# Kernel optimization log

Hardware: AMD Instinct MI355X
Metric: run time of the kernel (lower is better)

The kernel has to match this reference:

```python
import jax, jax.numpy as jnp
import numpy as np

N = 100000
E = 1600000
IN_DIM = 256
HID = 128
HEADS = 8
DH = HID // HEADS  # 16
NCLS = 64
SLOPE = 0.2  # DGL GATConv default negative_slope


def gat_layer(h_in, W, al, ar, b, src, dst, n_nodes, heads, dh, activate):
    # per-node linear transform -> [N, H, D]
    h = (h_in @ W).reshape(n_nodes, heads, dh)
    el = jnp.sum(h * al, axis=-1)  # [N, H]
    er = jnp.sum(h * ar, axis=-1)  # [N, H]
    e = jax.nn.leaky_relu(el[src] + er[dst], SLOPE)  # [E, H]
    # edge softmax over incoming edges of each dst node (numerically stable)
    m = jax.ops.segment_max(e, dst, num_segments=n_nodes)  # [N, H]
    m = jnp.where(jnp.isfinite(m), m, jnp.zeros_like(m))  # zero-in-degree nodes
    p = jnp.exp(e - m[dst])
    s = jax.ops.segment_sum(p, dst, num_segments=n_nodes)  # [N, H]
    alpha = p / s[dst]  # [E, H]
    # gather src features, weight by attention, scatter-add to dst
    msg = h[src] * alpha[..., None]  # [E, H, D]
    out = jax.ops.segment_sum(msg, dst, num_segments=n_nodes)  # [N, H, D]
    out = out + b.reshape(1, heads, dh)
    return jax.nn.elu(out) if activate else out


def setup_inputs() -> dict:
    key = jax.random.key(0)
    ks = jax.random.split(key, 12)
    x = jax.random.normal(ks[0], (N, IN_DIM), dtype=jnp.float32)
    src = jax.random.randint(ks[1], (E,), 0, N, dtype=jnp.int32)
    dst = jax.random.randint(ks[2], (E,), 0, N, dtype=jnp.int32)
    s1 = 1.0 / np.sqrt(IN_DIM)
    s2 = 1.0 / np.sqrt(HID)
    W1 = jax.random.normal(ks[3], (IN_DIM, HID), dtype=jnp.float32) * s1
    al1 = jax.random.normal(ks[4], (HEADS, DH), dtype=jnp.float32) * s2
    ar1 = jax.random.normal(ks[5], (HEADS, DH), dtype=jnp.float32) * s2
    b1 = jnp.zeros((HID,), dtype=jnp.float32)
    W2 = jax.random.normal(ks[6], (HID, NCLS), dtype=jnp.float32) * s2
    al2 = jax.random.normal(ks[7], (1, NCLS), dtype=jnp.float32) * s2
    ar2 = jax.random.normal(ks[8], (1, NCLS), dtype=jnp.float32) * s2
    b2 = jnp.zeros((NCLS,), dtype=jnp.float32)
    return {"x": x, "src": src, "dst": dst, "W1": W1, "al1": al1, "ar1": ar1,
            "b1": b1, "W2": W2, "al2": al2, "ar2": ar2, "b2": b2}


def reference(x, src, dst, W1, al1, ar1, b1, W2, al2, ar2, b2):
    # Layer 1: 8-head GATConv with internal ELU activation
    h = gat_layer(x, W1, al1, ar1, b1, src, dst, N, HEADS, DH, activate=True)
    h = h.reshape(N, HID)  # concat heads
    h = jax.nn.elu(h)       # outer ELU (dropout is identity in eval)
    # Layer 2: single-head GATConv, no activation; mean over head dim
    out = gat_layer(h, W2, al2, ar2, b2, src, dst, N, 1, NCLS, activate=False)
    return out.mean(axis=1)  # [N, NCLS]
```

## Files before the change

### kernel.cpp

```cpp
#include <hip/hip_runtime.h>
#include <hip/hip_bf16.h>
#include <cstdint>
#include <cstddef>

#define NNODES 100000
#define NEDGES 1600000
#define IN_DIM 256
#define HID 128
#define HEADS 8
#define DH 16
#define NCLS 64
#define SLOPE 0.2f

#define NBUCK 391
#define BCAP 5120
#define EPB 4000
#define NBBLK 400

typedef __attribute__((ext_vector_type(8))) short bf16x8;
typedef __attribute__((ext_vector_type(4))) float f32x4;

static __device__ __forceinline__ unsigned short f2bf(float f) {
    __hip_bfloat16 h = __float2bfloat16(f);
    unsigned short r;
    __builtin_memcpy(&r, &h, sizeof(r));
    return r;
}
static __device__ __forceinline__ float bflo(unsigned int w) {
    union { uint32_t u; float f; } c; c.u = w << 16; return c.f;
}
static __device__ __forceinline__ float bfhi(unsigned int w) {
    union { uint32_t u; float f; } c; c.u = w & 0xFFFF0000u; return c.f;
}

__global__ __launch_bounds__(256) void prep_w1t_kernel(const float* __restrict__ W1,
                                                       short* __restrict__ W1T) {
    int idx = blockIdx.x * 256 + threadIdx.x;
    if (idx >= IN_DIM * HID) return;
    int k = idx >> 7;
    int n = idx & 127;
    W1T[n * IN_DIM + k] = (short)f2bf(W1[idx]);
}

__global__ __launch_bounds__(256) void prep_w2t_kernel(const float* __restrict__ W2,
                                                       short* __restrict__ W2T) {
    int idx = blockIdx.x * 256 + threadIdx.x;
    if (idx >= HID * NCLS) return;
    int k = idx >> 6;
    int n = idx & 63;
    W2T[n * HID + k] = (short)f2bf(W2[idx]);
}

__global__ __launch_bounds__(256) void gemm1_kernel(const float* __restrict__ x,
                                                    const short* __restrict__ W1T,
                                                    unsigned short* __restrict__ h1b) {
    __shared__ short Asl[128 * 40];
    const int tid = threadIdx.x;
    const int brow = blockIdx.x * 128;
    const int wid = tid >> 6, lane = tid & 63;
    const int wm = (wid >> 1) * 64, wn = (wid & 1) * 64;
    const int mr = lane & 15;
    const int ks = lane >> 4;
    const int sr = tid >> 1;
    const int sch = tid & 1;
    const int grow = brow + sr;
    const bool rowok = grow < NNODES;
    const float* xrow = x + (size_t)grow * IN_DIM + sch * 16;

    f32x4 acc[4][4];
#pragma unroll
    for (int i = 0; i < 4; ++i)
#pragma unroll
        for (int j = 0; j < 4; ++j) acc[i][j] = (f32x4){0.f, 0.f, 0.f, 0.f};

    float4 v0 = {0,0,0,0}, v1 = {0,0,0,0}, v2 = {0,0,0,0}, v3 = {0,0,0,0};
    if (rowok) {
        v0 = *(const float4*)(xrow + 0);
        v1 = *(const float4*)(xrow + 4);
        v2 = *(const float4*)(xrow + 8);
        v3 = *(const float4*)(xrow + 12);
    }

    for (int k0 = 0; k0 < IN_DIM; k0 += 32) {
        bf16x8 p0, p1;
        p0[0] = (short)f2bf(v0.x); p0[1] = (short)f2bf(v0.y);
        p0[2] = (short)f2bf(v0.z); p0[3] = (short)f2bf(v0.w);
        p0[4] = (short)f2bf(v1.x); p0[5] = (short)f2bf(v1.y);
        p0[6] = (short)f2bf(v1.z); p0[7] = (short)f2bf(v1.w);
        p1[0] = (short)f2bf(v2.x); p1[1] = (short)f2bf(v2.y);
        p1[2] = (short)f2bf(v2.z); p1[3] = (short)f2bf(v2.w);
        p1[4] = (short)f2bf(v3.x); p1[5] = (short)f2bf(v3.y);
        p1[6] = (short)f2bf(v3.z); p1[7] = (short)f2bf(v3.w);
        if (k0 + 32 < IN_DIM && rowok) {
            v0 = *(const float4*)(xrow + k0 + 32 + 0);
            v1 = *(const float4*)(xrow + k0 + 32 + 4);
            v2 = *(const float4*)(xrow + k0 + 32 + 8);
            v3 = *(const float4*)(xrow + k0 + 32 + 12);
        }
        __syncthreads();
        *(bf16x8*)(Asl + sr * 40 + sch * 16 + 0) = p0;
        *(bf16x8*)(Asl + sr * 40 + sch * 16 + 8) = p1;
        __syncthreads();

        bf16x8 af[4], bfr[4];
#pragma unroll
        for (int i = 0; i < 4; ++i)
            af[i] = *(const bf16x8*)(Asl + (wm + i * 16 + mr) * 40 + ks * 8);
#pragma unroll
        for (int j = 0; j < 4; ++j)
            bfr[j] = *(const bf16x8*)(W1T + (size_t)(wn + j * 16 + mr) * IN_DIM + k0 + ks * 8);
#pragma unroll
        for (int i = 0; i < 4; ++i)
#pragma unroll
            for (int j = 0; j < 4; ++j)
                acc[i][j] = __builtin_amdgcn_mfma_f32_16x16x32_bf16(af[i], bfr[j], acc[i][j], 0, 0, 0);
    }

#pragma unroll
    for (int i = 0; i < 4; ++i) {
#pragma unroll
        for (int j = 0; j < 4; ++j) {
            int col = wn + j * 16 + mr;
#pragma unroll
            for (int r = 0; r < 4; ++r) {
                int row = brow + wm + i * 16 + ks * 4 + r;
                if (row < NNODES) h1b[(size_t)row * HID + col] = f2bf(acc[i][j][r]);
            }
        }
    }
}

__global__ __launch_bounds__(256) void gemm2_kernel(const unsigned short* __restrict__ hfb,
                                                    const short* __restrict__ W2T,
                                                    const float* __restrict__ al2,
                                                    const float* __restrict__ ar2,
                                                    unsigned short* __restrict__ h2b,
                                                    float* __restrict__ el2,
                                                    float* __restrict__ er2) {
    __shared__ short A[128 * 136];
    const int tid = threadIdx.x;
    const int brow = blockIdx.x * 128;
    {
        int r = tid >> 1, half = tid & 1;
        int grow = brow + r;
        uint4* lp = (uint4*)(A + r * 136 + half * 64);
        if (grow < NNODES) {
            const uint4* gp = (const uint4*)(hfb + (size_t)grow * HID + half * 64);
#pragma unroll
            for (int i = 0; i < 8; ++i) lp[i] = gp[i];
        } else {
            uint4 z = {0, 0, 0, 0};
#pragma unroll
            for (int i = 0; i < 8; ++i) lp[i] = z;
        }
    }
    __syncthreads();

    const int wid = tid >> 6, lane = tid & 63;
    const int mr = lane & 15, ks = lane >> 4;
    const int wrow = wid * 32;

    f32x4 acc[2][4];
#pragma unroll
    for (int i = 0; i < 2; ++i)
#pragma unroll
        for (int j = 0; j < 4; ++j) acc[i][j] = (f32x4){0.f, 0.f, 0.f, 0.f};

#pragma unroll
    for (int kk = 0; kk < 4; ++kk) {
        const int k0 = kk * 32;
        bf16x8 af[2], bfr[4];
#pragma unroll
        for (int i = 0; i < 2; ++i)
            af[i] = *(const bf16x8*)(A + (wrow + i * 16 + mr) * 136 + k0 + ks * 8);
#pragma unroll
        for (int j = 0; j < 4; ++j)
            bfr[j] = *(const bf16x8*)(W2T + (size_t)(j * 16 + mr) * HID + k0 + ks * 8);
#pragma unroll
        for (int i = 0; i < 2; ++i)
#pragma unroll
            for (int j = 0; j < 4; ++j)
                acc[i][j] = __builtin_amdgcn_mfma_f32_16x16x32_bf16(af[i], bfr[j], acc[i][j], 0, 0, 0);
    }

    float al2v[4], ar2v[4];
#pragma unroll
    for (int j = 0; j < 4; ++j) { al2v[j] = al2[j * 16 + mr]; ar2v[j] = ar2[j * 16 + mr]; }

    float pl[2][4] = {}, pr[2][4] = {};
#pragma unroll
    for (int i = 0; i < 2; ++i) {
#pragma unroll
        for (int j = 0; j < 4; ++j) {
#pragma unroll
            for (int r = 0; r < 4; ++r) {
                float vvv = acc[i][j][r];
                pl[i][r] = fmaf(vvv, al2v[j], pl[i][r]);
                pr[i][r] = fmaf(vvv, ar2v[j], pr[i][r]);
                int row = brow + wrow + i * 16 + ks * 4 + r;
                if (row < NNODES) h2b[(size_t)row * NCLS + j * 16 + mr] = f2bf(vvv);
            }
        }
    }
#pragma unroll
    for (int d = 1; d <= 8; d <<= 1) {
#pragma unroll
        for (int i = 0; i < 2; ++i)
#pragma unroll
            for (int r = 0; r < 4; ++r) {
                pl[i][r] += __shfl_xor(pl[i][r], d, 64);
                pr[i][r] += __shfl_xor(pr[i][r], d, 64);
            }
    }
    if (mr == 0) {
#pragma unroll
        for (int i = 0; i < 2; ++i)
#pragma unroll
            for (int r = 0; r < 4; ++r) {
                int row = brow + wrow + i * 16 + ks * 4 + r;
                if (row < NNODES) { el2[row] = pl[i][r]; er2[row] = pr[i][r]; }
            }
    }
}

__global__ __launch_bounds__(256) void init_gcur_kernel(int* __restrict__ gcur) {
    int b = blockIdx.x * 256 + threadIdx.x;
    if (b < NBUCK) gcur[b] = b * BCAP;
}

__global__ __launch_bounds__(256) void bucket_scatter_kernel(const int* __restrict__ src,
                                                             const int* __restrict__ dst,
                                                             int* __restrict__ gcur,
                                                             unsigned* __restrict__ pairs) {
    __shared__ int cnt[NBUCK];
    __shared__ int base[NBUCK];
    const int tid = threadIdx.x;
    for (int i = tid; i < NBUCK; i += 256) cnt[i] = 0;
    __syncthreads();
    const int eb = blockIdx.x * EPB;
    for (int i = tid; i < EPB; i += 256) atomicAdd(&cnt[dst[eb + i] >> 8], 1);
    __syncthreads();
    for (int b = tid; b < NBUCK; b += 256) {
        int c = cnt[b];
        base[b] = c ? atomicAdd(&gcur[b], c) : 0;
        cnt[b] = 0;
    }
    __syncthreads();
    for (int i = tid; i < EPB; i += 256) {
        int d = dst[eb + i], s = src[eb + i];
        int b = d >> 8;
        int p = base[b] + atomicAdd(&cnt[b], 1);
        pairs[p] = ((unsigned)(d & 255) << 24) | (unsigned)s;
    }
}

__global__ __launch_bounds__(256) void bucket_csr_kernel(const unsigned* __restrict__ pairs,
                                                         const int* __restrict__ gcur,
                                                         int* __restrict__ row_off,
                                                         int* __restrict__ row_cnt,
                                                         int* __restrict__ sorted_src) {
    __shared__ int ncnt[256];
    __shared__ int nbase[256];
    __shared__ int ws[4];
    const int tid = threadIdx.x, lane = tid & 63, wid = tid >> 6;
    const int b = blockIdx.x;
    const int nbeg = b << 8;
    const int ebeg = b * BCAP;
    const int eend = gcur[b];

    ncnt[tid] = 0;
    __syncthreads();
    for (int pos = ebeg + tid; pos < eend; pos += 256)
        atomicAdd(&ncnt[pairs[pos] >> 24], 1);
    __syncthreads();
    int v = ncnt[tid];
    int x = v;
#pragma unroll
    for (int d = 1; d < 64; d <<= 1) {
        int y = __shfl_up(x, d, 64);
        if (lane >= d) x += y;
    }
    if (lane == 63) ws[wid] = x;
    __syncthreads();
    int woff = 0;
#pragma unroll
    for (int i = 0; i < 4; ++i) if (i < wid) woff += ws[i];
    int gb = ebeg + woff + (x - v);
    int node = nbeg + tid;
    if (node < NNODES) { row_off[node] = gb; row_cnt[node] = v; }
    nbase[tid] = gb;
    ncnt[tid] = 0;
    __syncthreads();
    for (int pos = ebeg + tid; pos < eend; pos += 256) {
        unsigned pr = pairs[pos];
        int l = pr >> 24;
        int p = nbase[l] + atomicAdd(&ncnt[l], 1);
        sorted_src[p] = (int)(pr & 0xFFFFFFu);
    }
}

__global__ __launch_bounds__(256) void attn_scores_kernel(const unsigned short* __restrict__ h1b,
                                                          const float* __restrict__ al,
                                                          const float* __restrict__ ar,
                                                          float* __restrict__ el,
                                                          float* __restrict__ er) {
    int idx = blockIdx.x * 256 + threadIdx.x;
    if (idx >= NNODES * HEADS) return;
    int hd = idx & (HEADS - 1);
    const uint4* hp = (const uint4*)(h1b + (size_t)idx * DH);
    uint4 A = hp[0], B = hp[1];
    unsigned int w[8] = {A.x, A.y, A.z, A.w, B.x, B.y, B.z, B.w};
    float a = 0.f, c = 0.f;
#pragma unroll
    for (int i = 0; i < 8; ++i) {
        float lo = bflo(w[i]), hi = bfhi(w[i]);
        a = fmaf(lo, al[hd * DH + 2 * i], a);
        a = fmaf(hi, al[hd * DH + 2 * i + 1], a);
        c = fmaf(lo, ar[hd * DH + 2 * i], c);
        c = fmaf(hi, ar[hd * DH + 2 * i + 1], c);
    }
    el[idx] = a;
    er[idx] = c;
}

__global__ __launch_bounds__(256) void aggregate1_kernel(const unsigned short* __restrict__ h1b,
                                                         const float* __restrict__ el1,
                                                         const float* __restrict__ er1,
                                                         const int* __restrict__ row_off,
                                                         const int* __restrict__ row_cnt,
                                                         const int* __restrict__ sorted_src,
                                                         const float* __restrict__ b1,
                                                         unsigned short* __restrict__ hfb) {
    __shared__ float b1s[HID];
    const int tid = threadIdx.x;
    if (tid < HID) b1s[tid] = b1[tid];
    __syncthreads();

    const int wid = tid >> 6, lane = tid & 63;
    const int g = lane >> 4, sub = lane & 15, hd = sub >> 1;

    for (int v = blockIdx.x * 4 + wid; v < NNODES; v += gridDim.x * 4) {
        const int beg = row_off[v];
        const int end = beg + row_cnt[v];
        const float er_v = er1[v * HEADS + hd];
        float a[8] = {0.f, 0.f, 0.f, 0.f, 0.f, 0.f, 0.f, 0.f};
        float sp = 0.f;
        for (int j0 = beg; j0 < end; j0 += 64) {
            const int nj = min(64, end - j0);
            const int nit = (nj + 3) >> 2;
            int us = (j0 + lane < end) ? sorted_src[j0 + lane] : 0;
            for (int ib = 0; ib < nit; ib += 4) {
                int j0i = g + 4 * (ib + 0), j1i = g + 4 * (ib + 1);
                int j2i = g + 4 * (ib + 2), j3i = g + 4 * (ib + 3);
                int u0 = __shfl(us, j0i, 64);
                int u1 = __shfl(us, j1i, 64);
                int u2 = __shfl(us, j2i, 64);
                int u3 = __shfl(us, j3i, 64);
                uint4 w0 = *(const uint4*)(h1b + ((unsigned)(u0 << 7) + sub * 8));
                uint4 w1 = *(const uint4*)(h1b + ((unsigned)(u1 << 7) + sub * 8));
                uint4 w2 = *(const uint4*)(h1b + ((unsigned)(u2 << 7) + sub * 8));
                uint4 w3 = *(const uint4*)(h1b + ((unsigned)(u3 << 7) + sub * 8));
                float e0 = el1[(unsigned)(u0 << 3) + hd];
                float e1 = el1[(unsigned)(u1 << 3) + hd];
                float e2 = el1[(unsigned)(u2 << 3) + hd];
                float e3 = el1[(unsigned)(u3 << 3) + hd];
                float s0 = e0 + er_v; s0 = s0 > 0.f ? s0 : SLOPE * s0;
                float s1 = e1 + er_v; s1 = s1 > 0.f ? s1 : SLOPE * s1;
                float s2 = e2 + er_v; s2 = s2 > 0.f ? s2 : SLOPE * s2;
                float s3 = e3 + er_v; s3 = s3 > 0.f ? s3 : SLOPE * s3;
                float p0 = (j0i < nj) ? __expf(s0) : 0.f;
                float p1 = (j1i < nj) ? __expf(s1) : 0.f;
                float p2 = (j2i < nj) ? __expf(s2) : 0.f;
                float p3 = (j3i < nj) ? __expf(s3) : 0.f;
                sp += p0 + p1 + p2 + p3;
#define ACC8(P, W) \
                a[0] = fmaf(P, bflo(W.x), a[0]); a[1] = fmaf(P, bfhi(W.x), a[1]); \
                a[2] = fmaf(P, bflo(W.y), a[2]); a[3] = fmaf(P, bfhi(W.y), a[3]); \
                a[4] = fmaf(P, bflo(W.z), a[4]); a[5] = fmaf(P, bfhi(W.z), a[5]); \
                a[6] = fmaf(P, bflo(W.w), a[6]); a[7] = fmaf(P, bfhi(W.w), a[7]);
                ACC8(p0, w0) ACC8(p1, w1) ACC8(p2, w2) ACC8(p3, w3)
#undef ACC8
            }
        }
#pragma unroll
        for (int d = 16; d <= 32; d <<= 1) {
#pragma unroll
            for (int i = 0; i < 8; ++i) a[i] += __shfl_xor(a[i], d, 64);
            sp += __shfl_xor(sp, d, 64);
        }
        float inv = sp > 0.f ? 1.0f / sp : 0.f;
        float f[8];
#pragma unroll
        for (int i = 0; i < 8; ++i) {
            float t = a[i] * inv + b1s[sub * 8 + i];
            t = t > 0.f ? t : __expf(t) - 1.f;
            t = t > 0.f ? t : __expf(t) - 1.f;
            f[i] = t;
        }
        if (g == 0) {
            uint4 w;
            w.x = (unsigned)f2bf(f[0]) | ((unsigned)f2bf(f[1]) << 16);
            w.y = (unsigned)f2bf(f[2]) | ((unsigned)f2bf(f[3]) << 16);
            w.z = (unsigned)f2bf(f[4]) | ((unsigned)f2bf(f[5]) << 16);
            w.w = (unsigned)f2bf(f[6]) | ((unsigned)f2bf(f[7]) << 16);
            *(uint4*)(hfb + (size_t)v * HID + sub * 8) = w;
        }
    }
}

__global__ __launch_bounds__(256) void aggregate2_kernel(const unsigned short* __restrict__ h2b,
                                                         const float* __restrict__ el2,
                                                         const float* __restrict__ er2,
                                                         const int* __restrict__ row_off,
                                                         const int* __restrict__ row_cnt,
                                                         const int* __restrict__ sorted_src,
                                                         const float* __restrict__ b2,
                                                         float* __restrict__ out) {
    const int tid = threadIdx.x;
    const int v = blockIdx.x * 4 + (tid >> 6);
    if (v >= NNODES) return;
    const int lane = tid & 63, g = lane >> 3, sub = lane & 7;
    const int beg = row_off[v];
    const int end = beg + row_cnt[v];
    const float er_v = er2[v];
    float a[8] = {0.f, 0.f, 0.f, 0.f, 0.f, 0.f, 0.f, 0.f};
    float sp = 0.f;
    for (int j0 = beg; j0 < end; j0 += 64) {
        const int nj = min(64, end - j0);
        const int nit = (nj + 7) >> 3;
        bool valid = j0 + lane < end;
        int us = valid ? sorted_src[j0 + lane] : 0;
        float ev = valid ? el2[us] : 0.f;
        for (int ib = 0; ib < nit; ib += 4) {
            int j0i = g + 8 * (ib + 0), j1i = g + 8 * (ib + 1);
            int j2i = g + 8 * (ib + 2), j3i = g + 8 * (ib + 3);
            int u0 = __shfl(us, j0i, 64);
            int u1 = __shfl(us, j1i, 64);
            int u2 = __shfl(us, j2i, 64);
            int u3 = __shfl(us, j3i, 64);
            float s0 = __shfl(ev, j0i, 64) + er_v; s0 = s0 > 0.f ? s0 : SLOPE * s0;
            float s1 = __shfl(ev, j1i, 64) + er_v; s1 = s1 > 0.f ? s1 : SLOPE * s1;
            float s2 = __shfl(ev, j2i, 64) + er_v; s2 = s2 > 0.f ? s2 : SLOPE * s2;
            float s3 = __shfl(ev, j3i, 64) + er_v; s3 = s3 > 0.f ? s3 : SLOPE * s3;
            float p0 = (j0i < nj) ? __expf(s0) : 0.f;
            float p1 = (j1i < nj) ? __expf(s1) : 0.f;
            float p2 = (j2i < nj) ? __expf(s2) : 0.f;
            float p3 = (j3i < nj) ? __expf(s3) : 0.f;
            uint4 w0 = *(const uint4*)(h2b + ((unsigned)(u0 << 6) + sub * 8));
            uint4 w1 = *(const uint4*)(h2b + ((unsigned)(u1 << 6) + sub * 8));
            uint4 w2 = *(const uint4*)(h2b + ((unsigned)(u2 << 6) + sub * 8));
            uint4 w3 = *(const uint4*)(h2b + ((unsigned)(u3 << 6) + sub * 8));
            sp += p0 + p1 + p2 + p3;
#define ACC8(P, W) \
            a[0] = fmaf(P, bflo(W.x), a[0]); a[1] = fmaf(P, bfhi(W.x), a[1]); \
            a[2] = fmaf(P, bflo(W.y), a[2]); a[3] = fmaf(P, bfhi(W.y), a[3]); \
            a[4] = fmaf(P, bflo(W.z), a[4]); a[5] = fmaf(P, bfhi(W.z), a[5]); \
            a[6] = fmaf(P, bflo(W.w), a[6]); a[7] = fmaf(P, bfhi(W.w), a[7]);
            ACC8(p0, w0) ACC8(p1, w1) ACC8(p2, w2) ACC8(p3, w3)
#undef ACC8
        }
    }
#pragma unroll
    for (int d = 8; d <= 32; d <<= 1) {
#pragma unroll
        for (int i = 0; i < 8; ++i) a[i] += __shfl_xor(a[i], d, 64);
        sp += __shfl_xor(sp, d, 64);
    }
    if (g == 0) {
        float inv = sp > 0.f ? 1.0f / sp : 0.f;
        float4 b0 = *(const float4*)(b2 + sub * 8);
        float4 b1v = *(const float4*)(b2 + sub * 8 + 4);
        float4 o0, o1;
        o0.x = a[0] * inv + b0.x; o0.y = a[1] * inv + b0.y;
        o0.z = a[2] * inv + b0.z; o0.w = a[3] * inv + b0.w;
        o1.x = a[4] * inv + b1v.x; o1.y = a[5] * inv + b1v.y;
        o1.z = a[6] * inv + b1v.z; o1.w = a[7] * inv + b1v.w;
        *(float4*)(out + (size_t)v * NCLS + sub * 8) = o0;
        *(float4*)(out + (size_t)v * NCLS + sub * 8 + 4) = o1;
    }
}

extern "C" void kernel_launch(void* const* d_in, const int* in_sizes, int n_in,
                              void* d_out, int out_size, void* d_ws, size_t ws_size,
                              hipStream_t stream) {
    const float* x   = (const float*)d_in[0];
    const int*   src = (const int*)d_in[1];
    const int*   dst = (const int*)d_in[2];
    const float* W1  = (const float*)d_in[3];
    const float* al1 = (const float*)d_in[4];
    const float* ar1 = (const float*)d_in[5];
    const float* b1  = (const float*)d_in[6];
    const float* W2  = (const float*)d_in[7];
    const float* al2 = (const float*)d_in[8];
    const float* ar2 = (const float*)d_in[9];
    const float* b2  = (const float*)d_in[10];
    float* out = (float*)d_out;

    float* el1 = (float*)d_ws;
    float* er1 = el1 + (size_t)NNODES * HEADS;
    float* el2 = er1 + (size_t)NNODES * HEADS;
    float* er2 = el2 + NNODES;
    unsigned short* h1b = (unsigned short*)(er2 + NNODES);
    unsigned short* hfb = h1b + (size_t)NNODES * HID;
    unsigned short* h2b = hfb + (size_t)NNODES * HID;
    int* row_off    = (int*)(h2b + (size_t)NNODES * NCLS);
    int* row_cnt    = row_off + NNODES + 4;
    int* sorted_src = row_cnt + NNODES;
    short* W1T      = (short*)(sorted_src + NBUCK * BCAP);
    short* W2T      = W1T + (size_t)HID * IN_DIM;
    int* gcur       = (int*)(W2T + (size_t)NCLS * HID);
    unsigned* pairs = (unsigned*)(gcur + NBUCK + 1);

    init_gcur_kernel<<<(NBUCK + 255) / 256, 256, 0, stream>>>(gcur);
    bucket_scatter_kernel<<<NBBLK, 256, 0, stream>>>(src, dst, gcur, pairs);
    bucket_csr_kernel<<<NBUCK, 256, 0, stream>>>(pairs, gcur, row_off, row_cnt, sorted_src);

    prep_w1t_kernel<<<(IN_DIM * HID + 255) / 256, 256, 0, stream>>>(W1, W1T);
    prep_w2t_kernel<<<(HID * NCLS + 255) / 256, 256, 0, stream>>>(W2, W2T);
    gemm1_kernel<<<(NNODES + 127) / 128, 256, 0, stream>>>(x, W1T, h1b);
    attn_scores_kernel<<<(NNODES * HEADS + 255) / 256, 256, 0, stream>>>(h1b, al1, ar1, el1, er1);
    aggregate1_kernel<<<2048, 256, 0, stream>>>(h1b, el1, er1, row_off, row_cnt, sorted_src,
                                                b1, hfb);

    gemm2_kernel<<<(NNODES + 127) / 128, 256, 0, stream>>>(hfb, W2T, al2, ar2, h2b, el2, er2);
    aggregate2_kernel<<<(NNODES + 3) / 4, 256, 0, stream>>>(h2b, el2, er2, row_off, row_cnt,
                                                            sorted_src, b2, out);
}
```

Measured before the change: 261.0 us.

## Merge independent preprocessing and GEMM kernels into combined heterogeneous-block launches

Independent kernels are merged into three launches whose blocks are split by blockIdx. The first does weight transposes plus bucket-cursor init. The second runs edge bucket scattering alongside the first GEMM, and the third runs CSR construction alongside attention-score computation. This cuts the launch count from eight to three and lets the independent graph-preprocessing and dense work overlap on the GPU. In exchange, the shared-memory footprint of the combined kernels is the larger of the two roles, and block-level load imbalance between the roles may limit the overlap.

```diff
diff --git a/kernel.cpp b/kernel.cpp
--- a/kernel.cpp
+++ b/kernel.cpp
@@ -16,6 +16,8 @@
 #define BCAP 5120
 #define EPB 4000
 #define NBBLK 400
+#define G1BLK 782
+#define ATTNBLK 3125
 
 typedef __attribute__((ext_vector_type(8))) short bf16x8;
 typedef __attribute__((ext_vector_type(4))) float f32x4;
@@ -33,30 +35,60 @@
     union { uint32_t u; float f; } c; c.u = w & 0xFFFF0000u; return c.f;
 }
 
-__global__ __launch_bounds__(256) void prep_w1t_kernel(const float* __restrict__ W1,
-                                                       short* __restrict__ W1T) {
+__global__ __launch_bounds__(256) void stage0_prep_kernel(const float* __restrict__ W1,
+                                                          const float* __restrict__ W2,
+                                                          short* __restrict__ W1T,
+                                                          short* __restrict__ W2T,
+                                                          int* __restrict__ gcur) {
     int idx = blockIdx.x * 256 + threadIdx.x;
-    if (idx >= IN_DIM * HID) return;
-    int k = idx >> 7;
-    int n = idx & 127;
-    W1T[n * IN_DIM + k] = (short)f2bf(W1[idx]);
-}
-
-__global__ __launch_bounds__(256) void prep_w2t_kernel(const float* __restrict__ W2,
-                                                       short* __restrict__ W2T) {
-    int idx = blockIdx.x * 256 + threadIdx.x;
-    if (idx >= HID * NCLS) return;
-    int k = idx >> 6;
-    int n = idx & 63;
-    W2T[n * HID + k] = (short)f2bf(W2[idx]);
-}
-
-__global__ __launch_bounds__(256) void gemm1_kernel(const float* __restrict__ x,
-                                                    const short* __restrict__ W1T,
-                                                    unsigned short* __restrict__ h1b) {
-    __shared__ short Asl[128 * 40];
+    if (idx < IN_DIM * HID) {
+        int k = idx >> 7, n = idx & 127;
+        W1T[n * IN_DIM + k] = (short)f2bf(W1[idx]);
+    } else if (idx < IN_DIM * HID + HID * NCLS) {
+        int j = idx - IN_DIM * HID;
+        int k = j >> 6, n = j & 63;
+        W2T[n * HID + k] = (short)f2bf(W2[j]);
+    } else {
+        int b = idx - IN_DIM * HID - HID * NCLS;
+        if (b < NBUCK) gcur[b] = b * BCAP;
+    }
+}
+
+__global__ __launch_bounds__(256) void stage1_kernel(const int* __restrict__ src,
+                                                     const int* __restrict__ dst,
+                                                     int* __restrict__ gcur,
+                                                     unsigned* __restrict__ pairs,
+                                                     const float* __restrict__ x,
+                                                     const short* __restrict__ W1T,
+                                                     unsigned short* __restrict__ h1b) {
+    __shared__ __align__(16) char smem[128 * 40 * 2];
     const int tid = threadIdx.x;
-    const int brow = blockIdx.x * 128;
+
+    if (blockIdx.x < NBBLK) {
+        int* cnt  = (int*)smem;
+        int* base = cnt + NBUCK;
+        for (int i = tid; i < NBUCK; i += 256) cnt[i] = 0;
+        __syncthreads();
+        const int eb = blockIdx.x * EPB;
+        for (int i = tid; i < EPB; i += 256) atomicAdd(&cnt[dst[eb + i] >> 8], 1);
+        __syncthreads();
+        for (int b = tid; b < NBUCK; b += 256) {
+            int c = cnt[b];
+            base[b] = c ? atomicAdd(&gcur[b], c) : 0;
+            cnt[b] = 0;
+        }
+        __syncthreads();
+        for (int i = tid; i < EPB; i += 256) {
+            int d = dst[eb + i], s = src[eb + i];
+            int b = d >> 8;
+            int p = base[b] + atomicAdd(&cnt[b], 1);
+            pairs[p] = ((unsigned)(d & 255) << 24) | (unsigned)s;
+        }
+        return;
+    }
+
+    short* Asl = (short*)smem;
+    const int brow = (blockIdx.x - NBBLK) * 128;
     const int wid = tid >> 6, lane = tid & 63;
     const int wm = (wid >> 1) * 64, wn = (wid & 1) * 64;
     const int mr = lane & 15;
@@ -128,6 +160,79 @@
             }
         }
     }
+}
+
+__global__ __launch_bounds__(256) void stage2_kernel(const unsigned* __restrict__ pairs,
+                                                     const int* __restrict__ gcur,
+                                                     int* __restrict__ row_off,
+                                                     int* __restrict__ row_cnt,
+                                                     int* __restrict__ sorted_src,
+                                                     const unsigned short* __restrict__ h1b,
+                                                     const float* __restrict__ al,
+                                                     const float* __restrict__ ar,
+                                                     float* __restrict__ el,
+                                                     float* __restrict__ er) {
+    __shared__ int ncnt[256];
+    __shared__ int nbase[256];
+    __shared__ int ws[4];
+    const int tid = threadIdx.x;
+
+    if (blockIdx.x < NBUCK) {
+        const int lane = tid & 63, wid = tid >> 6;
+        const int b = blockIdx.x;
+        const int nbeg = b << 8;
+        const int ebeg = b * BCAP;
+        const int eend = gcur[b];
+
+        ncnt[tid] = 0;
+        __syncthreads();
+        for (int pos = ebeg + tid; pos < eend; pos += 256)
+            atomicAdd(&ncnt[pairs[pos] >> 24], 1);
+        __syncthreads();
+        int v = ncnt[tid];
+        int x = v;
+#pragma unroll
+        for (int d = 1; d < 64; d <<= 1) {
+            int y = __shfl_up(x, d, 64);
+            if (lane >= d) x += y;
+        }
+        if (lane == 63) ws[wid] = x;
+        __syncthreads();
+        int woff = 0;
+#pragma unroll
+        for (int i = 0; i < 4; ++i) if (i < wid) woff += ws[i];
+        int gb = ebeg + woff + (x - v);
+        int node = nbeg + tid;
+        if (node < NNODES) { row_off[node] = gb; row_cnt[node] = v; }
+        nbase[tid] = gb;
+        ncnt[tid] = 0;
+        __syncthreads();
+        for (int pos = ebeg + tid; pos < eend; pos += 256) {
+            unsigned pr = pairs[pos];
+            int l = pr >> 24;
+            int p = nbase[l] + atomicAdd(&ncnt[l], 1);
+            sorted_src[p] = (int)(pr & 0xFFFFFFu);
+        }
+        return;
+    }
+
+    int idx = (blockIdx.x - NBUCK) * 256 + tid;
+    if (idx >= NNODES * HEADS) return;
+    int hd = idx & (HEADS - 1);
+    const uint4* hp = (const uint4*)(h1b + (size_t)idx * DH);
+    uint4 A = hp[0], B = hp[1];
+    unsigned int w[8] = {A.x, A.y, A.z, A.w, B.x, B.y, B.z, B.w};
+    float a = 0.f, c = 0.f;
+#pragma unroll
+    for (int i = 0; i < 8; ++i) {
+        float lo = bflo(w[i]), hi = bfhi(w[i]);
+        a = fmaf(lo, al[hd * DH + 2 * i], a);
+        a = fmaf(hi, al[hd * DH + 2 * i + 1], a);
+        c = fmaf(lo, ar[hd * DH + 2 * i], c);
+        c = fmaf(hi, ar[hd * DH + 2 * i + 1], c);
+    }
+    el[idx] = a;
+    er[idx] = c;
 }
 
 __global__ __launch_bounds__(256) void gemm2_kernel(const unsigned short* __restrict__ hfb,
@@ -221,106 +326,6 @@
                 if (row < NNODES) { el2[row] = pl[i][r]; er2[row] = pr[i][r]; }
             }
     }
-}
-
-__global__ __launch_bounds__(256) void init_gcur_kernel(int* __restrict__ gcur) {
-    int b = blockIdx.x * 256 + threadIdx.x;
-    if (b < NBUCK) gcur[b] = b * BCAP;
-}
-
-__global__ __launch_bounds__(256) void bucket_scatter_kernel(const int* __restrict__ src,
-                                                             const int* __restrict__ dst,
-                                                             int* __restrict__ gcur,
-                                                             unsigned* __restrict__ pairs) {
-    __shared__ int cnt[NBUCK];
-    __shared__ int base[NBUCK];
-    const int tid = threadIdx.x;
-    for (int i = tid; i < NBUCK; i += 256) cnt[i] = 0;
-    __syncthreads();
-    const int eb = blockIdx.x * EPB;
-    for (int i = tid; i < EPB; i += 256) atomicAdd(&cnt[dst[eb + i] >> 8], 1);
-    __syncthreads();
-    for (int b = tid; b < NBUCK; b += 256) {
-        int c = cnt[b];
-        base[b] = c ? atomicAdd(&gcur[b], c) : 0;
-        cnt[b] = 0;
-    }
-    __syncthreads();
-    for (int i = tid; i < EPB; i += 256) {
-        int d = dst[eb + i], s = src[eb + i];
-        int b = d >> 8;
-        int p = base[b] + atomicAdd(&cnt[b], 1);
-        pairs[p] = ((unsigned)(d & 255) << 24) | (unsigned)s;
-    }
-}
-
-__global__ __launch_bounds__(256) void bucket_csr_kernel(const unsigned* __restrict__ pairs,
-                                                         const int* __restrict__ gcur,
-                                                         int* __restrict__ row_off,
-                                                         int* __restrict__ row_cnt,
-                                                         int* __restrict__ sorted_src) {
-    __shared__ int ncnt[256];
-    __shared__ int nbase[256];
-    __shared__ int ws[4];
-    const int tid = threadIdx.x, lane = tid & 63, wid = tid >> 6;
-    const int b = blockIdx.x;
-    const int nbeg = b << 8;
-    const int ebeg = b * BCAP;
-    const int eend = gcur[b];
-
-    ncnt[tid] = 0;
-    __syncthreads();
-    for (int pos = ebeg + tid; pos < eend; pos += 256)
-        atomicAdd(&ncnt[pairs[pos] >> 24], 1);
-    __syncthreads();
-    int v = ncnt[tid];
-    int x = v;
-#pragma unroll
-    for (int d = 1; d < 64; d <<= 1) {
-        int y = __shfl_up(x, d, 64);
-        if (lane >= d) x += y;
-    }
-    if (lane == 63) ws[wid] = x;
-    __syncthreads();
-    int woff = 0;
-#pragma unroll
-    for (int i = 0; i < 4; ++i) if (i < wid) woff += ws[i];
-    int gb = ebeg + woff + (x - v);
-    int node = nbeg + tid;
-    if (node < NNODES) { row_off[node] = gb; row_cnt[node] = v; }
-    nbase[tid] = gb;
-    ncnt[tid] = 0;
-    __syncthreads();
-    for (int pos = ebeg + tid; pos < eend; pos += 256) {
-        unsigned pr = pairs[pos];
-        int l = pr >> 24;
-        int p = nbase[l] + atomicAdd(&ncnt[l], 1);
-        sorted_src[p] = (int)(pr & 0xFFFFFFu);
-    }
-}
-
-__global__ __launch_bounds__(256) void attn_scores_kernel(const unsigned short* __restrict__ h1b,
-                                                          const float* __restrict__ al,
-                                                          const float* __restrict__ ar,
-                                                          float* __restrict__ el,
-                                                          float* __restrict__ er) {
-    int idx = blockIdx.x * 256 + threadIdx.x;
-    if (idx >= NNODES * HEADS) return;
-    int hd = idx & (HEADS - 1);
-    const uint4* hp = (const uint4*)(h1b + (size_t)idx * DH);
-    uint4 A = hp[0], B = hp[1];
-    unsigned int w[8] = {A.x, A.y, A.z, A.w, B.x, B.y, B.z, B.w};
-    float a = 0.f, c = 0.f;
-#pragma unroll
-    for (int i = 0; i < 8; ++i) {
-        float lo = bflo(w[i]), hi = bfhi(w[i]);
-        a = fmaf(lo, al[hd * DH + 2 * i], a);
-        a = fmaf(hi, al[hd * DH + 2 * i + 1], a);
-        c = fmaf(lo, ar[hd * DH + 2 * i], c);
-        c = fmaf(hi, ar[hd * DH + 2 * i + 1], c);
-    }
-    el[idx] = a;
-    er[idx] = c;
 }
 
 __global__ __launch_bounds__(256) void aggregate1_kernel(const unsigned short* __restrict__ h1b,
@@ -511,14 +516,14 @@
     int* gcur       = (int*)(W2T + (size_t)NCLS * HID);
     unsigned* pairs = (unsigned*)(gcur + NBUCK + 1);
 
-    init_gcur_kernel<<<(NBUCK + 255) / 256, 256, 0, stream>>>(gcur);
-    bucket_scatter_kernel<<<NBBLK, 256, 0, stream>>>(src, dst, gcur, pairs);
-    bucket_csr_kernel<<<NBUCK, 256, 0, stream>>>(pairs, gcur, row_off, row_cnt, sorted_src);
-
-    prep_w1t_kernel<<<(IN_DIM * HID + 255) / 256, 256, 0, stream>>>(W1, W1T);
-    prep_w2t_kernel<<<(HID * NCLS + 255) / 256, 256, 0, stream>>>(W2, W2T);
-    gemm1_kernel<<<(NNODES + 127) / 128, 256, 0, stream>>>(x, W1T, h1b);
-    attn_scores_kernel<<<(NNODES * HEADS + 255) / 256, 256, 0, stream>>>(h1b, al1, ar1, el1, er1);
+    const int prep_total = IN_DIM * HID + HID * NCLS + NBUCK;
+    stage0_prep_kernel<<<(prep_total + 255) / 256, 256, 0, stream>>>(W1, W2, W1T, W2T, gcur);
+
+    stage1_kernel<<<NBBLK + G1BLK, 256, 0, stream>>>(src, dst, gcur, pairs, x, W1T, h1b);
+
+    stage2_kernel<<<NBUCK + ATTNBLK, 256, 0, stream>>>(pairs, gcur, row_off, row_cnt, sorted_src,
+                                                       h1b, al1, ar1, el1, er1);
+
     aggregate1_kernel<<<2048, 256, 0, stream>>>(h1b, el1, er1, row_off, row_cnt, sorted_src,
                                                 b1, hfb);
 
```

Result: faster. 244.5 us, median of 2 (-6.3%).
